# Performance work log

Hardware: AMD Instinct MI355X
Metric: run time of the kernel (lower is better)

The kernel has to match this reference:

```python
import jax, jax.numpy as jnp
import numpy as np

D = 1024
B, S = 4, 2048

def setup_inputs() -> dict:
    key = jax.random.key(0)
    ks = jax.random.split(key, 4)
    scale = 1.0 / np.sqrt(D)
    return {
        "x": jax.random.normal(ks[0], (B, S, D), dtype=jnp.float32),
        "Wq": jax.random.normal(ks[1], (D, D), dtype=jnp.float32) * scale,
        "bq": jnp.zeros((D,), jnp.float32),
        "Wk": jax.random.normal(ks[2], (D, D), dtype=jnp.float32) * scale,
        "bk": jnp.zeros((D,), jnp.float32),
        "Wv": jax.random.normal(ks[3], (D, D), dtype=jnp.float32) * scale,
        "bv": jnp.zeros((D,), jnp.float32),
    }

def reference(x, Wq, bq, Wk, bk, Wv, bv):
    # torch Linear: y = x @ W.T + b
    Q = jnp.einsum('bsd,ed->bse', x, Wq) + bq
    K = jnp.einsum('bsd,ed->bse', x, Wk) + bk
    V = jnp.einsum('bsd,ed->bse', x, Wv) + bv
    # NOTE: original scales by sqrt(K.shape[1]) == sqrt(seq_len), kept faithfully
    dk = K.shape[1]
    logits = jnp.einsum('bqd,bkd->bqk', Q, K) / jnp.sqrt(jnp.asarray(dk, Q.dtype))
    att = jax.nn.softmax(logits, axis=-1)
    return jnp.einsum('bqk,bkd->bqd', att, V)
```

## Files before the change

### kernel.cpp

```cpp
#include <hip/hip_runtime.h>


typedef unsigned short u16;
typedef unsigned int u32;
typedef __bf16 bf16x8 __attribute__((ext_vector_type(8)));
typedef float floatx4 __attribute__((ext_vector_type(4)));

__device__ __forceinline__ u16 f2bf(float f) {
    u32 u = __float_as_uint(f);
    u += 0x7fffu + ((u >> 16) & 1u);
    return (u16)(u >> 16);
}

__device__ __forceinline__ void g2lds16(const void* g, void* l) {
    __builtin_amdgcn_global_load_lds(
        (const __attribute__((address_space(1))) unsigned int*)g,
        (__attribute__((address_space(3))) unsigned int*)l,
        16, 0, 0);
}

__global__ __launch_bounds__(256)
void cvt_all(const float* __restrict__ x, const float* __restrict__ Wq,
             const float* __restrict__ Wk, const float* __restrict__ Wv,
             u16* __restrict__ xb, u16* __restrict__ wall)
{
    const int NX = 2097152;
    const int NW = 262144;
    int i = blockIdx.x * 256 + threadIdx.x;
    const float* src;
    u16* dst;
    int idx;
    if (i < NX) { src = x; dst = xb; idx = i; }
    else {
        int j = i - NX;
        dst = wall; idx = j;
        src = (j < NW) ? Wq : (j < 2 * NW) ? Wk : Wv;
        int jj = (j < NW) ? j : (j < 2 * NW) ? (j - NW) : (j - 2 * NW);
        float4 v = ((const float4*)src)[jj];
        ushort4 o;
        o.x = f2bf(v.x); o.y = f2bf(v.y); o.z = f2bf(v.z); o.w = f2bf(v.w);
        ((ushort4*)dst)[idx] = o;
        return;
    }
    float4 v = ((const float4*)src)[idx];
    ushort4 o;
    o.x = f2bf(v.x); o.y = f2bf(v.y); o.z = f2bf(v.z); o.w = f2bf(v.w);
    ((ushort4*)dst)[idx] = o;
}

template<int MODE>
__global__ __launch_bounds__(512, 2)
void gemm_big(const u16* __restrict__ A, const u16* __restrict__ B,
              void* __restrict__ Out, const float* __restrict__ bias,
              float scale, int M, int N, int K,
              long long sAz, long long sBz, long long sOz,
              void* __restrict__ Out2, void* __restrict__ Out3,
              const float* __restrict__ bias2, const float* __restrict__ bias3)
{
    __shared__ u16 ldsA[2][256 * 64];
    __shared__ u16 ldsB[2][256 * 64];

    const int tid   = threadIdx.x;
    const int lane  = tid & 63;
    const int wv    = tid >> 6;
    const int wm    = (wv >> 1) * 64;
    const int wn    = (wv & 1) * 128;
    const int lhalf = lane & 15;
    const int quad  = lane >> 4;

    const size_t bz = blockIdx.z;
    A += bz * (size_t)sAz;
    B += bz * (size_t)sBz;

    int tm, tn;
    {
        const int ntn = gridDim.x, ntm = gridDim.y;
        const int lin = blockIdx.y * ntn + blockIdx.x;
        const int GM = 4;
        const int width = GM * ntn;
        const int group = lin / width;
        const int first = group * GM;
        const int gsz   = (ntm - first) < GM ? (ntm - first) : GM;
        const int rem   = lin - group * width;
        tm = first + rem % gsz;
        tn = rem / gsz;
    }
    const int m0 = tm * 256;
    const int n0 = tn * 256;

    const int r8 = lane >> 3;
    const int gc = (lane & 7) ^ r8;
    const u16* pa = A + (size_t)(m0 + 8 * wv + r8) * K + gc * 8;
    const u16* pb = B + (size_t)(n0 + 8 * wv + r8) * K + gc * 8;
    const int lbase = wv * 512;

    floatx4 zero = {0.f, 0.f, 0.f, 0.f};
    floatx4 acc[4][8];
#pragma unroll
    for (int i = 0; i < 4; ++i)
#pragma unroll
        for (int j = 0; j < 8; ++j) acc[i][j] = zero;

    const int swz = lhalf & 7;

#pragma unroll
    for (int j = 0; j < 4; ++j) {
        g2lds16(pa + (size_t)(64 * j) * K, &ldsA[0][lbase + j * 4096]);
        g2lds16(pb + (size_t)(64 * j) * K, &ldsB[0][lbase + j * 4096]);
    }
    pa += 64; pb += 64;

    int buf = 0;
    for (int k0 = 0; k0 < K; k0 += 64) {
        __syncthreads();
        if (k0 + 64 < K) {
#pragma unroll
            for (int j = 0; j < 4; ++j) {
                g2lds16(pa + (size_t)(64 * j) * K, &ldsA[buf ^ 1][lbase + j * 4096]);
                g2lds16(pb + (size_t)(64 * j) * K, &ldsB[buf ^ 1][lbase + j * 4096]);
            }
            pa += 64; pb += 64;
        }

        const u16* lA = ldsA[buf];
        const u16* lB = ldsB[buf];
#pragma unroll
        for (int ks = 0; ks < 2; ++ks) {
            const int c = ks * 4 + quad;
            const int p = c ^ swz;
            bf16x8 af[4], bfv[8];
#pragma unroll
            for (int i = 0; i < 4; ++i)
                af[i] = *(const bf16x8*)(lA + (wm + i * 16 + lhalf) * 64 + p * 8);
#pragma unroll
            for (int j = 0; j < 8; ++j)
                bfv[j] = *(const bf16x8*)(lB + (wn + j * 16 + lhalf) * 64 + p * 8);
#pragma unroll
            for (int i = 0; i < 4; ++i)
#pragma unroll
                for (int j = 0; j < 8; ++j)
                    acc[i][j] = __builtin_amdgcn_mfma_f32_16x16x32_bf16(
                        af[i], bfv[j], acc[i][j], 0, 0, 0);
        }
        buf ^= 1;
    }

#pragma unroll
    for (int i = 0; i < 4; ++i) {
        const int mb = m0 + wm + i * 16 + quad * 4;
#pragma unroll
        for (int j = 0; j < 8; ++j) {
            const int n = n0 + wn + j * 16 + lhalf;
            if (MODE == 0) {
#pragma unroll
                for (int r = 0; r < 4; ++r)
                    ((u16*)Out)[bz * (size_t)sOz + (size_t)(mb + r) * N + n] =
                        f2bf(acc[i][j][r] * scale);
            } else if (MODE == 2) {
#pragma unroll
                for (int r = 0; r < 4; ++r)
                    ((float*)Out)[bz * (size_t)sOz + (size_t)(mb + r) * N + n] =
                        acc[i][j][r] * scale;
            } else {
                if (n < 1024) {
                    const float bb = bias[n];
#pragma unroll
                    for (int r = 0; r < 4; ++r)
                        ((u16*)Out)[(size_t)(mb + r) * 1024 + n] =
                            f2bf(acc[i][j][r] + bb);
                } else if (n < 2048) {
                    const float bb = bias2[n - 1024];
#pragma unroll
                    for (int r = 0; r < 4; ++r)
                        ((u16*)Out2)[(size_t)(mb + r) * 1024 + (n - 1024)] =
                            f2bf(acc[i][j][r] + bb);
                } else {
                    const int d = n - 2048;
                    const float bb = bias3[d];
                    const int b = mb >> 11;
                    const int s0 = mb & 2047;
                    ushort4 w;
                    w.x = f2bf(acc[i][j][0] + bb);
                    w.y = f2bf(acc[i][j][1] + bb);
                    w.z = f2bf(acc[i][j][2] + bb);
                    w.w = f2bf(acc[i][j][3] + bb);
                    *(ushort4*)((u16*)Out3 + (size_t)b * 2097152 +
                                (size_t)d * 2048 + s0) = w;
                }
            }
        }
    }
}

__global__ __launch_bounds__(256)
void softmax_rows(u16* __restrict__ S)
{
    const int tid = threadIdx.x;
    u16* row = S + (size_t)blockIdx.x * 2048;
    uint4 v = ((const uint4*)row)[tid];
    float x[8];
    x[0] = __uint_as_float(v.x << 16); x[1] = __uint_as_float(v.x & 0xffff0000u);
    x[2] = __uint_as_float(v.y << 16); x[3] = __uint_as_float(v.y & 0xffff0000u);
    x[4] = __uint_as_float(v.z << 16); x[5] = __uint_as_float(v.z & 0xffff0000u);
    x[6] = __uint_as_float(v.w << 16); x[7] = __uint_as_float(v.w & 0xffff0000u);

    float mx = x[0];
#pragma unroll
    for (int i = 1; i < 8; ++i) mx = fmaxf(mx, x[i]);
#pragma unroll
    for (int off = 32; off > 0; off >>= 1) mx = fmaxf(mx, __shfl_xor(mx, off, 64));

    __shared__ float sm[4], ss[4];
    if ((tid & 63) == 0) sm[tid >> 6] = mx;
    __syncthreads();
    mx = fmaxf(fmaxf(sm[0], sm[1]), fmaxf(sm[2], sm[3]));

    float e[8];
    float s = 0.f;
#pragma unroll
    for (int i = 0; i < 8; ++i) { e[i] = __expf(x[i] - mx); s += e[i]; }
#pragma unroll
    for (int off = 32; off > 0; off >>= 1) s += __shfl_xor(s, off, 64);
    if ((tid & 63) == 0) ss[tid >> 6] = s;
    __syncthreads();
    s = (ss[0] + ss[1]) + (ss[2] + ss[3]);

    const float inv = 1.f / s;
    uint4 o;
    o.x = (u32)f2bf(e[0] * inv) | ((u32)f2bf(e[1] * inv) << 16);
    o.y = (u32)f2bf(e[2] * inv) | ((u32)f2bf(e[3] * inv) << 16);
    o.z = (u32)f2bf(e[4] * inv) | ((u32)f2bf(e[5] * inv) << 16);
    o.w = (u32)f2bf(e[6] * inv) | ((u32)f2bf(e[7] * inv) << 16);
    ((uint4*)row)[tid] = o;
}

extern "C" void kernel_launch(void* const* d_in, const int* in_sizes, int n_in,
                              void* d_out, int out_size, void* d_ws, size_t ws_size,
                              hipStream_t stream)
{
    const float* x  = (const float*)d_in[0];
    const float* Wq = (const float*)d_in[1];
    const float* bq = (const float*)d_in[2];
    const float* Wk = (const float*)d_in[3];
    const float* bk = (const float*)d_in[4];
    const float* Wv = (const float*)d_in[5];
    const float* bv = (const float*)d_in[6];
    float* out = (float*)d_out;

    const int B = 4, S = 2048, D = 1024;
    const long long SD = (long long)S * D;
    const long long SS = (long long)S * S;
    const long long BSD = (long long)B * SD;
    const long long DD = (long long)D * D;

    u16* xb   = (u16*)d_ws;
    u16* wall = xb   + BSD;
    u16* Qb   = wall + 3 * DD;
    u16* Kb   = Qb   + BSD;
    u16* Vt   = Kb   + BSD;
    u16* Sc   = Vt   + BSD;

    cvt_all<<<dim3(11264), 256, 0, stream>>>(x, Wq, Wk, Wv, xb, wall);

    gemm_big<3><<<dim3(3 * D / 256, (B * S) / 256, 1), 512, 0, stream>>>(
        xb, wall, Qb, bq, 1.f, B * S, 3 * D, D, 0, 0, 0, Kb, Vt, bk, bv);

    const float sc = 0.022097086912079608f;
    gemm_big<0><<<dim3(S / 256, S / 256, B), 512, 0, stream>>>(
        Qb, Kb, Sc, nullptr, sc, S, S, D, SD, SD, SS,
        nullptr, nullptr, nullptr, nullptr);

    softmax_rows<<<dim3(B * S), 256, 0, stream>>>(Sc);

    gemm_big<2><<<dim3(D / 256, S / 256, B), 512, 0, stream>>>(
        Sc, Vt, out, nullptr, 1.f, S, D, S, SS, SD, SD,
        nullptr, nullptr, nullptr, nullptr);
}
```

Baseline: 294.3 us.

## Shrink GEMM tiles to 128x128 and switch to 32x32x16 MFMA

All three GEMMs now use 128x128 tiles with 256 threads (four waves, each computing 64x64) instead of 256x256 tiles with 512 threads. Each wave issues 32x32x16 bf16 MFMAs in place of 16x16x32, and the epilogue is rewritten for the 32x32 accumulator layout. The aim is more blocks for better CU fill (the QK^T and PV grids were small) plus a higher-throughput MFMA shape. The cost is lower operand reuse per LDS byte, more global traffic, and more scattered 2-byte epilogue stores.

```diff
diff --git a/kernel.cpp b/kernel.cpp
--- a/kernel.cpp
+++ b/kernel.cpp
@@ -4,7 +4,7 @@
 typedef unsigned short u16;
 typedef unsigned int u32;
 typedef __bf16 bf16x8 __attribute__((ext_vector_type(8)));
-typedef float floatx4 __attribute__((ext_vector_type(4)));
+typedef float floatx16 __attribute__((ext_vector_type(16)));
 
 __device__ __forceinline__ u16 f2bf(float f) {
     u32 u = __float_as_uint(f);
@@ -49,24 +49,24 @@
 }
 
 template<int MODE>
-__global__ __launch_bounds__(512, 2)
-void gemm_big(const u16* __restrict__ A, const u16* __restrict__ B,
-              void* __restrict__ Out, const float* __restrict__ bias,
-              float scale, int M, int N, int K,
-              long long sAz, long long sBz, long long sOz,
-              void* __restrict__ Out2, void* __restrict__ Out3,
-              const float* __restrict__ bias2, const float* __restrict__ bias3)
-{
-    __shared__ u16 ldsA[2][256 * 64];
-    __shared__ u16 ldsB[2][256 * 64];
+__global__ __launch_bounds__(256, 2)
+void gemm_bt(const u16* __restrict__ A, const u16* __restrict__ B,
+             void* __restrict__ Out, const float* __restrict__ bias,
+             float scale, int M, int N, int K,
+             long long sAz, long long sBz, long long sOz,
+             void* __restrict__ Out2, void* __restrict__ Out3,
+             const float* __restrict__ bias2, const float* __restrict__ bias3)
+{
+    __shared__ u16 ldsA[2][128 * 64];
+    __shared__ u16 ldsB[2][128 * 64];
 
     const int tid   = threadIdx.x;
     const int lane  = tid & 63;
     const int wv    = tid >> 6;
     const int wm    = (wv >> 1) * 64;
-    const int wn    = (wv & 1) * 128;
-    const int lhalf = lane & 15;
-    const int quad  = lane >> 4;
+    const int wn    = (wv & 1) * 64;
+    const int l31   = lane & 31;
+    const int khalf = lane >> 5;
 
     const size_t bz = blockIdx.z;
     A += bz * (size_t)sAz;
@@ -85,28 +85,29 @@
         tm = first + rem % gsz;
         tn = rem / gsz;
     }
-    const int m0 = tm * 256;
-    const int n0 = tn * 256;
+    const int m0 = tm * 128;
+    const int n0 = tn * 128;
 
     const int r8 = lane >> 3;
     const int gc = (lane & 7) ^ r8;
-    const u16* pa = A + (size_t)(m0 + 8 * wv + r8) * K + gc * 8;
-    const u16* pb = B + (size_t)(n0 + 8 * wv + r8) * K + gc * 8;
-    const int lbase = wv * 512;
-
-    floatx4 zero = {0.f, 0.f, 0.f, 0.f};
-    floatx4 acc[4][8];
-#pragma unroll
-    for (int i = 0; i < 4; ++i)
-#pragma unroll
-        for (int j = 0; j < 8; ++j) acc[i][j] = zero;
-
-    const int swz = lhalf & 7;
+    const u16* pa = A + (size_t)(m0 + wv * 32 + r8) * K + gc * 8;
+    const u16* pb = B + (size_t)(n0 + wv * 32 + r8) * K + gc * 8;
+    const int lofs = wv * 2048;
+
+    floatx16 acc[2][2];
+#pragma unroll
+    for (int i = 0; i < 2; ++i)
+#pragma unroll
+        for (int j = 0; j < 2; ++j)
+#pragma unroll
+            for (int r = 0; r < 16; ++r) acc[i][j][r] = 0.f;
+
+    const int swz = lane & 7;
 
 #pragma unroll
     for (int j = 0; j < 4; ++j) {
-        g2lds16(pa + (size_t)(64 * j) * K, &ldsA[0][lbase + j * 4096]);
-        g2lds16(pb + (size_t)(64 * j) * K, &ldsB[0][lbase + j * 4096]);
+        g2lds16(pa + (size_t)(j * 8) * K, &ldsA[0][lofs + j * 512]);
+        g2lds16(pb + (size_t)(j * 8) * K, &ldsB[0][lofs + j * 512]);
     }
     pa += 64; pb += 64;
 
@@ -116,8 +117,8 @@
         if (k0 + 64 < K) {
 #pragma unroll
             for (int j = 0; j < 4; ++j) {
-                g2lds16(pa + (size_t)(64 * j) * K, &ldsA[buf ^ 1][lbase + j * 4096]);
-                g2lds16(pb + (size_t)(64 * j) * K, &ldsB[buf ^ 1][lbase + j * 4096]);
+                g2lds16(pa + (size_t)(j * 8) * K, &ldsA[buf ^ 1][lofs + j * 512]);
+                g2lds16(pb + (size_t)(j * 8) * K, &ldsB[buf ^ 1][lofs + j * 512]);
             }
             pa += 64; pb += 64;
         }
@@ -125,67 +126,78 @@
         const u16* lA = ldsA[buf];
         const u16* lB = ldsB[buf];
 #pragma unroll
-        for (int ks = 0; ks < 2; ++ks) {
-            const int c = ks * 4 + quad;
+        for (int ks = 0; ks < 4; ++ks) {
+            const int c = ks * 2 + khalf;
             const int p = c ^ swz;
-            bf16x8 af[4], bfv[8];
-#pragma unroll
-            for (int i = 0; i < 4; ++i)
-                af[i] = *(const bf16x8*)(lA + (wm + i * 16 + lhalf) * 64 + p * 8);
-#pragma unroll
-            for (int j = 0; j < 8; ++j)
-                bfv[j] = *(const bf16x8*)(lB + (wn + j * 16 + lhalf) * 64 + p * 8);
-#pragma unroll
-            for (int i = 0; i < 4; ++i)
-#pragma unroll
-                for (int j = 0; j < 8; ++j)
-                    acc[i][j] = __builtin_amdgcn_mfma_f32_16x16x32_bf16(
+            bf16x8 af[2], bfv[2];
+#pragma unroll
+            for (int i = 0; i < 2; ++i)
+                af[i] = *(const bf16x8*)(lA + (wm + i * 32 + l31) * 64 + p * 8);
+#pragma unroll
+            for (int j = 0; j < 2; ++j)
+                bfv[j] = *(const bf16x8*)(lB + (wn + j * 32 + l31) * 64 + p * 8);
+#pragma unroll
+            for (int i = 0; i < 2; ++i)
+#pragma unroll
+                for (int j = 0; j < 2; ++j)
+                    acc[i][j] = __builtin_amdgcn_mfma_f32_32x32x16_bf16(
                         af[i], bfv[j], acc[i][j], 0, 0, 0);
         }
         buf ^= 1;
     }
 
 #pragma unroll
-    for (int i = 0; i < 4; ++i) {
-        const int mb = m0 + wm + i * 16 + quad * 4;
-#pragma unroll
-        for (int j = 0; j < 8; ++j) {
-            const int n = n0 + wn + j * 16 + lhalf;
+    for (int i = 0; i < 2; ++i) {
+        const int mbase = m0 + wm + i * 32 + 4 * khalf;
+#pragma unroll
+        for (int j = 0; j < 2; ++j) {
+            const int n = n0 + wn + j * 32 + l31;
             if (MODE == 0) {
 #pragma unroll
-                for (int r = 0; r < 4; ++r)
-                    ((u16*)Out)[bz * (size_t)sOz + (size_t)(mb + r) * N + n] =
+                for (int r = 0; r < 16; ++r) {
+                    const int m = mbase + (r & 3) + 8 * (r >> 2);
+                    ((u16*)Out)[bz * (size_t)sOz + (size_t)m * N + n] =
                         f2bf(acc[i][j][r] * scale);
+                }
             } else if (MODE == 2) {
 #pragma unroll
-                for (int r = 0; r < 4; ++r)
-                    ((float*)Out)[bz * (size_t)sOz + (size_t)(mb + r) * N + n] =
+                for (int r = 0; r < 16; ++r) {
+                    const int m = mbase + (r & 3) + 8 * (r >> 2);
+                    ((float*)Out)[bz * (size_t)sOz + (size_t)m * N + n] =
                         acc[i][j][r] * scale;
+                }
             } else {
                 if (n < 1024) {
                     const float bb = bias[n];
 #pragma unroll
-                    for (int r = 0; r < 4; ++r)
-                        ((u16*)Out)[(size_t)(mb + r) * 1024 + n] =
-                            f2bf(acc[i][j][r] + bb);
+                    for (int r = 0; r < 16; ++r) {
+                        const int m = mbase + (r & 3) + 8 * (r >> 2);
+                        ((u16*)Out)[(size_t)m * 1024 + n] = f2bf(acc[i][j][r] + bb);
+                    }
                 } else if (n < 2048) {
                     const float bb = bias2[n - 1024];
 #pragma unroll
-                    for (int r = 0; r < 4; ++r)
-                        ((u16*)Out2)[(size_t)(mb + r) * 1024 + (n - 1024)] =
+                    for (int r = 0; r < 16; ++r) {
+                        const int m = mbase + (r & 3) + 8 * (r >> 2);
+                        ((u16*)Out2)[(size_t)m * 1024 + (n - 1024)] =
                             f2bf(acc[i][j][r] + bb);
+                    }
                 } else {
                     const int d = n - 2048;
                     const float bb = bias3[d];
-                    const int b = mb >> 11;
-                    const int s0 = mb & 2047;
-                    ushort4 w;
-                    w.x = f2bf(acc[i][j][0] + bb);
-                    w.y = f2bf(acc[i][j][1] + bb);
-                    w.z = f2bf(acc[i][j][2] + bb);
-                    w.w = f2bf(acc[i][j][3] + bb);
-                    *(ushort4*)((u16*)Out3 + (size_t)b * 2097152 +
-                                (size_t)d * 2048 + s0) = w;
+#pragma unroll
+                    for (int q = 0; q < 4; ++q) {
+                        const int m = mbase + 8 * q;
+                        const int b = m >> 11;
+                        const int s0 = m & 2047;
+                        ushort4 w;
+                        w.x = f2bf(acc[i][j][4 * q + 0] + bb);
+                        w.y = f2bf(acc[i][j][4 * q + 1] + bb);
+                        w.z = f2bf(acc[i][j][4 * q + 2] + bb);
+                        w.w = f2bf(acc[i][j][4 * q + 3] + bb);
+                        *(ushort4*)((u16*)Out3 + (size_t)b * 2097152 +
+                                    (size_t)d * 2048 + s0) = w;
+                    }
                 }
             }
         }
@@ -262,17 +274,17 @@
 
     cvt_all<<<dim3(11264), 256, 0, stream>>>(x, Wq, Wk, Wv, xb, wall);
 
-    gemm_big<3><<<dim3(3 * D / 256, (B * S) / 256, 1), 512, 0, stream>>>(
+    gemm_bt<3><<<dim3(3 * D / 128, (B * S) / 128, 1), 256, 0, stream>>>(
         xb, wall, Qb, bq, 1.f, B * S, 3 * D, D, 0, 0, 0, Kb, Vt, bk, bv);
 
     const float sc = 0.022097086912079608f;
-    gemm_big<0><<<dim3(S / 256, S / 256, B), 512, 0, stream>>>(
+    gemm_bt<0><<<dim3(S / 128, S / 128, B), 256, 0, stream>>>(
         Qb, Kb, Sc, nullptr, sc, S, S, D, SD, SD, SS,
         nullptr, nullptr, nullptr, nullptr);
 
     softmax_rows<<<dim3(B * S), 256, 0, stream>>>(Sc);
 
-    gemm_big<2><<<dim3(D / 256, S / 256, B), 512, 0, stream>>>(
+    gemm_bt<2><<<dim3(D / 128, S / 128, B), 256, 0, stream>>>(
         Sc, Vt, out, nullptr, 1.f, S, D, S, SS, SD, SD,
         nullptr, nullptr, nullptr, nullptr);
 }
```

Result: faster. 264.0 us (-10.3%).
